# Optimization experiments

Hardware: AMD Instinct MI355X
Metric: run time of the kernel (lower is better)

Reference implementation:

```python
import jax, jax.numpy as jnp
import numpy as np

NUM_HEADS = 16
HEAD_SIZE = 64
HIDDEN = NUM_HEADS * HEAD_SIZE  # 1024


def setup_inputs() -> dict:
    key = jax.random.key(0)
    ks = jax.random.split(key, 9)
    B, S1, S2 = 8, 1024, 1024
    scale = 1.0 / np.sqrt(HIDDEN)
    inp = {
        "s1_hidden_states": jax.random.normal(ks[0], (B, S1, HIDDEN), jnp.float32),
        "s2_hidden_states": jax.random.normal(ks[1], (B, S2, HIDDEN), jnp.float32),
        "s2_attention_mask": jnp.zeros((B, 1, 1, S2), jnp.float32),
        "Wq": jax.random.normal(ks[2], (HIDDEN, HIDDEN), jnp.float32) * scale,
        "bq": jnp.zeros((HIDDEN,), jnp.float32),
        "Wk": jax.random.normal(ks[3], (HIDDEN, HIDDEN), jnp.float32) * scale,
        "bk": jnp.zeros((HIDDEN,), jnp.float32),
        "Wv": jax.random.normal(ks[4], (HIDDEN, HIDDEN), jnp.float32) * scale,
        "bv": jnp.zeros((HIDDEN,), jnp.float32),
        "cl_att": 1,
    }
    return inp


def _split_heads(x):
    # [B, S, H*D] -> [B, H, S, D]
    B, S, _ = x.shape
    return x.reshape(B, S, NUM_HEADS, HEAD_SIZE).transpose(0, 2, 1, 3)


def reference(s1_hidden_states, s2_hidden_states, s2_attention_mask,
              Wq, bq, Wk, bk, Wv, bv, cl_att):
    q = _split_heads(s1_hidden_states @ Wq + bq)  # [B,H,S1,D]
    k = _split_heads(s2_hidden_states @ Wk + bk)  # [B,H,S2,D]
    v = _split_heads(s2_hidden_states @ Wv + bv)  # [B,H,S2,D]

    scores = jnp.einsum("bhqd,bhkd->bhqk", q, k) / np.sqrt(HEAD_SIZE)
    scores = scores + s2_attention_mask  # broadcast [B,1,1,S2]
    probs = jax.nn.softmax(scores, axis=-1)
    if cl_att:
        probs = jax.nn.softmax(1.0 - probs + s2_attention_mask, axis=-1)
    # dropout is identity in eval/reference mode
    ctx = jnp.einsum("bhqk,bhkd->bhqd", probs, v)  # [B,H,S1,D]
    B, _, S1, _ = ctx.shape
    return ctx.transpose(0, 2, 1, 3).reshape(B, S1, HIDDEN)
```

## Files before the change

### kernel.cpp

```cpp
#include <hip/hip_runtime.h>
#include <hip/hip_bf16.h>

typedef unsigned short u16;
typedef __attribute__((ext_vector_type(8))) short bf16x8;
typedef __attribute__((ext_vector_type(4))) float f32x4;
typedef __attribute__((ext_vector_type(4))) unsigned u32x4;

#define L2E 1.4426950408889634f

__device__ __forceinline__ u16 f2bf(float f) {
  unsigned u = __float_as_uint(f);
  u = u + 0x7fffu + ((u >> 16) & 1u);
  return (u16)(u >> 16);
}
__device__ __forceinline__ unsigned cvtpk(float a, float b) {
  unsigned r;
  asm("v_cvt_pk_bf16_f32 %0, %1, %2" : "=v"(r) : "v"(a), "v"(b));
  return r;
}

__global__ void conv_f32_bf16(const float* __restrict__ in, u16* __restrict__ out, int n4) {
  int i = blockIdx.x * blockDim.x + threadIdx.x;
  int stride = gridDim.x * blockDim.x;
  for (; i < n4; i += stride) {
    float4 v = ((const float4*)in)[i];
    ushort4 o = make_ushort4(f2bf(v.x), f2bf(v.y), f2bf(v.z), f2bf(v.w));
    ((ushort4*)out)[i] = o;
  }
}

__global__ void wtrans3(const float* __restrict__ Wq, const float* __restrict__ Wk,
                        const float* __restrict__ Wv,
                        u16* __restrict__ Wtq, u16* __restrict__ Wtk, u16* __restrict__ Wtv) {
  int z = blockIdx.z;
  const float* W = (z == 0) ? Wq : (z == 1) ? Wk : Wv;
  u16* Wt = (z == 0) ? Wtq : (z == 1) ? Wtk : Wtv;
  __shared__ float T[32][33];
  int k0 = blockIdx.y * 32, n0 = blockIdx.x * 32;
  int tx = threadIdx.x, ty = threadIdx.y;
  #pragma unroll
  for (int j = 0; j < 4; ++j) T[ty + 8*j][tx] = W[(size_t)(k0 + ty + 8*j) * 1024 + n0 + tx];
  __syncthreads();
  #pragma unroll
  for (int j = 0; j < 4; ++j) Wt[(size_t)(n0 + ty + 8*j) * 1024 + k0 + tx] = f2bf(T[tx][ty + 8*j]);
}

__global__ __launch_bounds__(256) void qkv_gemm3(const u16* __restrict__ X1, const u16* __restrict__ X2,
                                                 const u16* __restrict__ Wtq, const u16* __restrict__ Wtk,
                                                 const u16* __restrict__ Wtv,
                                                 const float* __restrict__ bq, const float* __restrict__ bk,
                                                 const float* __restrict__ bv,
                                                 u16* __restrict__ Qo, u16* __restrict__ Ko, u16* __restrict__ Vo) {
  int z = blockIdx.z;
  const u16* X   = (z == 0) ? X1 : X2;
  const u16* Wt  = (z == 0) ? Wtq : (z == 1) ? Wtk : Wtv;
  const float* bias = (z == 0) ? bq : (z == 1) ? bk : bv;
  u16* outp = (z == 0) ? Qo : (z == 1) ? Ko : Vo;

  __shared__ __align__(16) u16 As[128 * 32];
  __shared__ __align__(16) u16 Bs[128 * 32];
  int tid = threadIdx.x;
  int m0 = blockIdx.y * 128, n0 = blockIdx.x * 128;
  int w = tid >> 6, l = tid & 63;
  int wm = w >> 1, wn = w & 1;
  const int4* Xs = (const int4*)X;
  const int4* Ws = (const int4*)Wt;
  int4* As4 = (int4*)As;
  int4* Bs4 = (int4*)Bs;
  f32x4 acc[4][4] = {};
  for (int kt = 0; kt < 32; ++kt) {
    #pragma unroll
    for (int c = 0; c < 2; ++c) {
      int i = c * 256 + tid;
      int row = i >> 2, kc = i & 3;
      __builtin_amdgcn_global_load_lds(
          (const __attribute__((address_space(1))) void*)&Xs[(size_t)(m0 + row) * 128 + kt * 4 + kc],
          (__attribute__((address_space(3))) void*)&As4[i], 16, 0, 0);
      __builtin_amdgcn_global_load_lds(
          (const __attribute__((address_space(1))) void*)&Ws[(size_t)(n0 + row) * 128 + kt * 4 + kc],
          (__attribute__((address_space(3))) void*)&Bs4[i], 16, 0, 0);
    }
    __syncthreads();
    bf16x8 a[4], bb[4];
    #pragma unroll
    for (int mc = 0; mc < 4; ++mc) a[mc]  = *(const bf16x8*)&As[(wm*64 + mc*16 + (l & 15)) * 32 + (l >> 4) * 8];
    #pragma unroll
    for (int nc = 0; nc < 4; ++nc) bb[nc] = *(const bf16x8*)&Bs[(wn*64 + nc*16 + (l & 15)) * 32 + (l >> 4) * 8];
    #pragma unroll
    for (int mc = 0; mc < 4; ++mc)
      #pragma unroll
      for (int nc = 0; nc < 4; ++nc)
        acc[mc][nc] = __builtin_amdgcn_mfma_f32_16x16x32_bf16(a[mc], bb[nc], acc[mc][nc], 0, 0, 0);
    __syncthreads();
  }
  #pragma unroll
  for (int nc = 0; nc < 4; ++nc) {
    int n = n0 + wn * 64 + nc * 16 + (l & 15);
    float bvv = bias[n];
    int h = n >> 6, d = n & 63;
    #pragma unroll
    for (int mc = 0; mc < 4; ++mc) {
      int srow_base = m0 + wm * 64 + mc * 16 + (l >> 4) * 4;
      if (z == 2) {
        int b = srow_base >> 10, s = srow_base & 1023;
        ushort4 vv;
        vv.x = f2bf(acc[mc][nc][0] + bvv);
        vv.y = f2bf(acc[mc][nc][1] + bvv);
        vv.z = f2bf(acc[mc][nc][2] + bvv);
        vv.w = f2bf(acc[mc][nc][3] + bvv);
        *(ushort4*)&outp[((size_t)((b * 16 + h) * 64 + d)) * 1024 + s] = vv;
      } else {
        #pragma unroll
        for (int r = 0; r < 4; ++r) {
          int sm = srow_base + r;
          int b = sm >> 10, s = sm & 1023;
          outp[((size_t)((b * 16 + h) * 1024 + s)) * 64 + d] = f2bf(acc[mc][nc][r] + bvv);
        }
      }
    }
  }
}

__global__ __launch_bounds__(256, 3) void attn12(const u16* __restrict__ Q, const u16* __restrict__ K,
                                                 const u16* __restrict__ Vt, const float* __restrict__ mask,
                                                 const int* __restrict__ clp, float* __restrict__ out) {
  __shared__ __align__(16) u16 KVl[2][8192];
  __shared__ __align__(16) float maskL2[1024];
  __shared__ float z1p[4][32];
  __shared__ float z2p[4][32];

  int bid = blockIdx.x;
  int xcd = bid & 7, idx = bid >> 3;
  int bh = xcd * 16 + (idx >> 5);
  int qt = idx & 31;
  int b = bh >> 4, h = bh & 15;
  int tid = threadIdx.x;
  int w = tid >> 6, l = tid & 63;
  int lq = l & 15, g = l >> 4;
  int qb = qt * 32;

  const u16* Kb = K + (size_t)bh * 65536;
  const u16* Vb = Vt + (size_t)bh * 65536;
  int cl = clp[0];

  const u16* kS[4]; int kD[4];
  #pragma unroll
  for (int c_ = 0; c_ < 4; ++c_) {
    int i_ = c_ * 256 + tid, row_ = i_ >> 3, ch_ = i_ & 7;
    int f_ = (row_ & 3) | ((((row_ >> 3) ^ (row_ >> 4)) & 1) << 2);
    kS[c_] = Kb + row_ * 64 + (ch_ ^ f_) * 8;
    kD[c_] = i_ * 8;
  }
  const u16* vS[4]; int vD[4];
  #pragma unroll
  for (int c_ = 0; c_ < 4; ++c_) {
    int i_ = c_ * 256 + tid, row_ = i_ >> 4, ch_ = i_ & 15;
    vS[c_] = Vb + row_ * 1024 + (ch_ ^ (row_ & 15)) * 8;
    vD[c_] = i_ * 8;
  }

#define STAGE_K(bi, t) do { _Pragma("unroll")                                                 \
    for (int c_ = 0; c_ < 4; ++c_)                                                           \
      __builtin_amdgcn_global_load_lds(                                                      \
        (const __attribute__((address_space(1))) void*)(kS[c_] + (t) * 8192),                \
        (__attribute__((address_space(3))) void*)&KVl[bi][kD[c_]], 16, 0, 0); } while (0)

#define STAGE_V(bi, t) do { _Pragma("unroll")                                                 \
    for (int c_ = 0; c_ < 4; ++c_)                                                           \
      __builtin_amdgcn_global_load_lds(                                                      \
        (const __attribute__((address_space(1))) void*)(vS[c_] + (t) * 128),                 \
        (__attribute__((address_space(3))) void*)&KVl[bi][vD[c_]], 16, 0, 0); } while (0)

  STAGE_K(0, 0);

  for (int i = tid; i < 1024; i += 256) maskL2[i] = mask[b * 1024 + i] * L2E;

  bf16x8 qf[2][2];
  #pragma unroll
  for (int qg = 0; qg < 2; ++qg) {
    const u16* Qp = Q + ((size_t)bh * 1024 + qb + qg * 16 + lq) * 64 + g * 8;
    qf[qg][0] = *(const bf16x8*)Qp;
    qf[qg][1] = *(const bf16x8*)(Qp + 32);
  }

  int kOff[2][2];
  #pragma unroll
  for (int c = 0; c < 2; ++c) {
    int row128 = w * 32 + ((lq >> 2) << 3) + c * 4 + (lq & 3);
    int F = (row128 & 3) | ((((row128 >> 3) ^ (row128 >> 4)) & 1) << 2);
    kOff[c][0] = row128 * 64 + ((g ^ F) * 8);
    kOff[c][1] = row128 * 64 + (((g + 4) ^ F) * 8);
  }
  int vOff[4];
  #pragma unroll
  for (int dc = 0; dc < 4; ++dc) {
    int row = dc * 16 + lq;
    vOff[dc] = row * 128 + (((w * 4 + g) ^ (row & 15)) * 8);
  }
  int mBase = w * 32 + g * 8;

  __syncthreads();

  const float sl2e = 0.125f * L2E;
  float z1[2] = {0.f, 0.f};
  int cur = 0;
  #pragma unroll
  for (int t = 0; t < 8; ++t) {
    if (t < 7) STAGE_K(cur ^ 1, t + 1);
    else       STAGE_K(0, 0);
    #pragma unroll
    for (int c = 0; c < 2; ++c) {
      bf16x8 kf0 = *(const bf16x8*)&KVl[cur][kOff[c][0]];
      bf16x8 kf1 = *(const bf16x8*)&KVl[cur][kOff[c][1]];
      const float4 mk = *(const float4*)&maskL2[t * 128 + mBase + c * 4];
      #pragma unroll
      for (int qg = 0; qg < 2; ++qg) {
        f32x4 tt = {0.f, 0.f, 0.f, 0.f};
        tt = __builtin_amdgcn_mfma_f32_16x16x32_bf16(kf0, qf[qg][0], tt, 0, 0, 0);
        tt = __builtin_amdgcn_mfma_f32_16x16x32_bf16(kf1, qf[qg][1], tt, 0, 0, 0);
        float e0 = __builtin_amdgcn_exp2f(fmaf(tt[0], sl2e, mk.x));
        float e1 = __builtin_amdgcn_exp2f(fmaf(tt[1], sl2e, mk.y));
        float e2 = __builtin_amdgcn_exp2f(fmaf(tt[2], sl2e, mk.z));
        float e3 = __builtin_amdgcn_exp2f(fmaf(tt[3], sl2e, mk.w));
        z1[qg] += (e0 + e1) + (e2 + e3);
      }
    }
    __syncthreads();
    cur ^= 1;
  }
  STAGE_V(1, 0);

  #pragma unroll
  for (int qg = 0; qg < 2; ++qg) {
    z1[qg] += __shfl_xor(z1[qg], 16);
    z1[qg] += __shfl_xor(z1[qg], 32);
  }
  if (l < 16) { z1p[w][l] = z1[0]; z1p[w][16 + l] = z1[1]; }
  __syncthreads();
  float lm[2];
  #pragma unroll
  for (int qg = 0; qg < 2; ++qg) {
    int q = qg * 16 + lq;
    lm[qg] = __builtin_amdgcn_logf(((z1p[0][q] + z1p[1][q]) + (z1p[2][q] + z1p[3][q])));
  }

  f32x4 acc[2][4] = {};
  float z2[2] = {0.f, 0.f};
  #pragma unroll
  for (int t = 0; t < 8; ++t) {
    u32x4 pk[2];
    #pragma unroll
    for (int c = 0; c < 2; ++c) {
      bf16x8 kf0 = *(const bf16x8*)&KVl[0][kOff[c][0]];
      bf16x8 kf1 = *(const bf16x8*)&KVl[0][kOff[c][1]];
      const float4 mk = *(const float4*)&maskL2[t * 128 + mBase + c * 4];
      #pragma unroll
      for (int qg = 0; qg < 2; ++qg) {
        f32x4 tt = {0.f, 0.f, 0.f, 0.f};
        tt = __builtin_amdgcn_mfma_f32_16x16x32_bf16(kf0, qf[qg][0], tt, 0, 0, 0);
        tt = __builtin_amdgcn_mfma_f32_16x16x32_bf16(kf1, qf[qg][1], tt, 0, 0, 0);
        float p10 = __builtin_amdgcn_exp2f(fmaf(tt[0], sl2e, mk.x) - lm[qg]);
        float p11 = __builtin_amdgcn_exp2f(fmaf(tt[1], sl2e, mk.y) - lm[qg]);
        float p12 = __builtin_amdgcn_exp2f(fmaf(tt[2], sl2e, mk.z) - lm[qg]);
        float p13 = __builtin_amdgcn_exp2f(fmaf(tt[3], sl2e, mk.w) - lm[qg]);
        if (cl) {
          float p20 = __builtin_amdgcn_exp2f(fmaf(-L2E, p10, mk.x));
          float p21 = __builtin_amdgcn_exp2f(fmaf(-L2E, p11, mk.y));
          float p22 = __builtin_amdgcn_exp2f(fmaf(-L2E, p12, mk.z));
          float p23 = __builtin_amdgcn_exp2f(fmaf(-L2E, p13, mk.w));
          z2[qg] += (p20 + p21) + (p22 + p23);
          pk[qg][c * 2 + 0] = cvtpk(p20, p21);
          pk[qg][c * 2 + 1] = cvtpk(p22, p23);
        } else {
          pk[qg][c * 2 + 0] = cvtpk(p10, p11);
          pk[qg][c * 2 + 1] = cvtpk(p12, p13);
        }
      }
    }
    #pragma unroll
    for (int dc = 0; dc < 4; ++dc) {
      bf16x8 vf = *(const bf16x8*)&KVl[1][vOff[dc]];
      #pragma unroll
      for (int qg = 0; qg < 2; ++qg)
        acc[qg][dc] = __builtin_amdgcn_mfma_f32_16x16x32_bf16(
            __builtin_bit_cast(bf16x8, pk[qg]), vf, acc[qg][dc], 0, 0, 0);
    }
    __syncthreads();
    if (t < 7) {
      STAGE_K(0, t + 1);
      STAGE_V(1, t + 1);
      __syncthreads();
    }
  }

  #pragma unroll
  for (int qg = 0; qg < 2; ++qg) {
    z2[qg] += __shfl_xor(z2[qg], 16);
    z2[qg] += __shfl_xor(z2[qg], 32);
  }
  if (l < 16) { z2p[w][l] = z2[0]; z2p[w][16 + l] = z2[1]; }
  float* redF = (float*)&KVl[0][0];
  if (w > 0) {
    #pragma unroll
    for (int qg = 0; qg < 2; ++qg)
      #pragma unroll
      for (int dc = 0; dc < 4; ++dc)
        #pragma unroll
        for (int r = 0; r < 4; ++r)
          redF[(w - 1) * 2176 + (qg * 16 + g * 4 + r) * 68 + dc * 16 + lq] = acc[qg][dc][r];
  }
  __syncthreads();
  if (w == 0) {
    #pragma unroll
    for (int qg = 0; qg < 2; ++qg) {
      #pragma unroll
      for (int r = 0; r < 4; ++r) {
        int q = qg * 16 + g * 4 + r;
        float Z2 = (z2p[0][q] + z2p[1][q]) + (z2p[2][q] + z2p[3][q]);
        float phi = cl ? __builtin_amdgcn_rcpf(Z2) : 1.0f;
        size_t orow = ((size_t)(b * 1024 + qb + q)) * 1024 + h * 64;
        #pragma unroll
        for (int dc = 0; dc < 4; ++dc) {
          int dq = q * 68 + dc * 16 + lq;
          float o = acc[qg][dc][r] + redF[dq] + redF[2176 + dq] + redF[4352 + dq];
          out[orow + dc * 16 + lq] = o * phi;
        }
      }
    }
  }
#undef STAGE_K
#undef STAGE_V
}

extern "C" void kernel_launch(void* const* d_in, const int* in_sizes, int n_in,
                              void* d_out, int out_size, void* d_ws, size_t ws_size,
                              hipStream_t stream) {
  const float* s1   = (const float*)d_in[0];
  const float* s2   = (const float*)d_in[1];
  const float* mask = (const float*)d_in[2];
  const float* Wq   = (const float*)d_in[3];
  const float* bq   = (const float*)d_in[4];
  const float* Wk   = (const float*)d_in[5];
  const float* bk   = (const float*)d_in[6];
  const float* Wv   = (const float*)d_in[7];
  const float* bv   = (const float*)d_in[8];
  const int*   cl   = (const int*)d_in[9];
  float* out = (float*)d_out;

  u16* ws  = (u16*)d_ws;
  const size_t M1 = 1024 * 1024;
  u16* X1  = ws;
  u16* X2  = ws + 8 * M1;
  u16* Wtq = ws + 16 * M1;
  u16* Wtk = Wtq + M1;
  u16* Wtv = Wtk + M1;
  u16* Qb  = Wtv + M1;
  u16* Kb  = Qb + 8 * M1;
  u16* Vtb = Kb + 8 * M1;

  conv_f32_bf16<<<2048, 256, 0, stream>>>(s1, X1, 2097152);
  conv_f32_bf16<<<2048, 256, 0, stream>>>(s2, X2, 2097152);
  wtrans3<<<dim3(32, 32, 3), dim3(32, 8), 0, stream>>>(Wq, Wk, Wv, Wtq, Wtk, Wtv);
  qkv_gemm3<<<dim3(8, 64, 3), 256, 0, stream>>>(X1, X2, Wtq, Wtk, Wtv, bq, bk, bv, Qb, Kb, Vtb);
  attn12<<<4096, 256, 0, stream>>>(Qb, Kb, Vtb, mask, cl, out);
}
```

Baseline: 212.6 us.

## Cache unnormalized score exponentials in registers instead of recomputing QK^T

The first pass over K now stores the exp'd scores as packed bf16 in a 64-entry register array. The second pass reuses them with a reciprocal of the row sum instead of redoing the QK^T MFMAs and exponentials. K staging in the second pass is dropped and V is double-buffered, so one barrier per tile is removed. This saves MFMA and exp work but costs many more VGPRs, which is why occupancy is lowered from 3 to 2 blocks. Using bf16-rounded probabilities before the second softmax adds some precision loss.

```diff
diff --git a/kernel.cpp b/kernel.cpp
--- a/kernel.cpp
+++ b/kernel.cpp
@@ -18,6 +18,8 @@
   asm("v_cvt_pk_bf16_f32 %0, %1, %2" : "=v"(r) : "v"(a), "v"(b));
   return r;
 }
+__device__ __forceinline__ float lo16(unsigned v) { return __uint_as_float(v << 16); }
+__device__ __forceinline__ float hi16(unsigned v) { return __uint_as_float(v & 0xffff0000u); }
 
 __global__ void conv_f32_bf16(const float* __restrict__ in, u16* __restrict__ out, int n4) {
   int i = blockIdx.x * blockDim.x + threadIdx.x;
@@ -121,7 +123,7 @@
   }
 }
 
-__global__ __launch_bounds__(256, 3) void attn12(const u16* __restrict__ Q, const u16* __restrict__ K,
+__global__ __launch_bounds__(256, 2) void attn13(const u16* __restrict__ Q, const u16* __restrict__ K,
                                                  const u16* __restrict__ Vt, const float* __restrict__ mask,
                                                  const int* __restrict__ clp, float* __restrict__ out) {
   __shared__ __align__(16) u16 KVl[2][8192];
@@ -202,12 +204,13 @@
   __syncthreads();
 
   const float sl2e = 0.125f * L2E;
+  unsigned sp[64];
   float z1[2] = {0.f, 0.f};
   int cur = 0;
   #pragma unroll
   for (int t = 0; t < 8; ++t) {
     if (t < 7) STAGE_K(cur ^ 1, t + 1);
-    else       STAGE_K(0, 0);
+    else       STAGE_V(0, 0);
     #pragma unroll
     for (int c = 0; c < 2; ++c) {
       bf16x8 kf0 = *(const bf16x8*)&KVl[cur][kOff[c][0]];
@@ -223,12 +226,13 @@
         float e2 = __builtin_amdgcn_exp2f(fmaf(tt[2], sl2e, mk.z));
         float e3 = __builtin_amdgcn_exp2f(fmaf(tt[3], sl2e, mk.w));
         z1[qg] += (e0 + e1) + (e2 + e3);
+        sp[t * 8 + qg * 4 + c * 2 + 0] = cvtpk(e0, e1);
+        sp[t * 8 + qg * 4 + c * 2 + 1] = cvtpk(e2, e3);
       }
     }
     __syncthreads();
     cur ^= 1;
   }
-  STAGE_V(1, 0);
 
   #pragma unroll
   for (int qg = 0; qg < 2; ++qg) {
@@ -237,60 +241,46 @@
   }
   if (l < 16) { z1p[w][l] = z1[0]; z1p[w][16 + l] = z1[1]; }
   __syncthreads();
-  float lm[2];
+  float cr[2];
   #pragma unroll
   for (int qg = 0; qg < 2; ++qg) {
     int q = qg * 16 + lq;
-    lm[qg] = __builtin_amdgcn_logf(((z1p[0][q] + z1p[1][q]) + (z1p[2][q] + z1p[3][q])));
+    float Z1 = (z1p[0][q] + z1p[1][q]) + (z1p[2][q] + z1p[3][q]);
+    cr[qg] = L2E * __builtin_amdgcn_rcpf(Z1);
   }
 
   f32x4 acc[2][4] = {};
   float z2[2] = {0.f, 0.f};
   #pragma unroll
   for (int t = 0; t < 8; ++t) {
+    if (t < 7) STAGE_V((t + 1) & 1, t + 1);
     u32x4 pk[2];
     #pragma unroll
-    for (int c = 0; c < 2; ++c) {
-      bf16x8 kf0 = *(const bf16x8*)&KVl[0][kOff[c][0]];
-      bf16x8 kf1 = *(const bf16x8*)&KVl[0][kOff[c][1]];
-      const float4 mk = *(const float4*)&maskL2[t * 128 + mBase + c * 4];
-      #pragma unroll
-      for (int qg = 0; qg < 2; ++qg) {
-        f32x4 tt = {0.f, 0.f, 0.f, 0.f};
-        tt = __builtin_amdgcn_mfma_f32_16x16x32_bf16(kf0, qf[qg][0], tt, 0, 0, 0);
-        tt = __builtin_amdgcn_mfma_f32_16x16x32_bf16(kf1, qf[qg][1], tt, 0, 0, 0);
-        float p10 = __builtin_amdgcn_exp2f(fmaf(tt[0], sl2e, mk.x) - lm[qg]);
-        float p11 = __builtin_amdgcn_exp2f(fmaf(tt[1], sl2e, mk.y) - lm[qg]);
-        float p12 = __builtin_amdgcn_exp2f(fmaf(tt[2], sl2e, mk.z) - lm[qg]);
-        float p13 = __builtin_amdgcn_exp2f(fmaf(tt[3], sl2e, mk.w) - lm[qg]);
-        if (cl) {
-          float p20 = __builtin_amdgcn_exp2f(fmaf(-L2E, p10, mk.x));
-          float p21 = __builtin_amdgcn_exp2f(fmaf(-L2E, p11, mk.y));
-          float p22 = __builtin_amdgcn_exp2f(fmaf(-L2E, p12, mk.z));
-          float p23 = __builtin_amdgcn_exp2f(fmaf(-L2E, p13, mk.w));
-          z2[qg] += (p20 + p21) + (p22 + p23);
-          pk[qg][c * 2 + 0] = cvtpk(p20, p21);
-          pk[qg][c * 2 + 1] = cvtpk(p22, p23);
-        } else {
-          pk[qg][c * 2 + 0] = cvtpk(p10, p11);
-          pk[qg][c * 2 + 1] = cvtpk(p12, p13);
+    for (int qg = 0; qg < 2; ++qg) {
+      if (cl) {
+        #pragma unroll
+        for (int j = 0; j < 4; ++j) {
+          unsigned e = sp[t * 8 + qg * 4 + j];
+          float mkA = maskL2[t * 128 + mBase + 2 * j];
+          float mkB = maskL2[t * 128 + mBase + 2 * j + 1];
+          float pA = __builtin_amdgcn_exp2f(fmaf(-cr[qg], lo16(e), mkA));
+          float pB = __builtin_amdgcn_exp2f(fmaf(-cr[qg], hi16(e), mkB));
+          z2[qg] += pA + pB;
+          pk[qg][j] = cvtpk(pA, pB);
         }
+      } else {
+        pk[qg] = *(u32x4*)&sp[t * 8 + qg * 4];
       }
     }
     #pragma unroll
     for (int dc = 0; dc < 4; ++dc) {
-      bf16x8 vf = *(const bf16x8*)&KVl[1][vOff[dc]];
+      bf16x8 vf = *(const bf16x8*)&KVl[t & 1][vOff[dc]];
       #pragma unroll
       for (int qg = 0; qg < 2; ++qg)
         acc[qg][dc] = __builtin_amdgcn_mfma_f32_16x16x32_bf16(
             __builtin_bit_cast(bf16x8, pk[qg]), vf, acc[qg][dc], 0, 0, 0);
     }
-    __syncthreads();
-    if (t < 7) {
-      STAGE_K(0, t + 1);
-      STAGE_V(1, t + 1);
-      __syncthreads();
-    }
+    if (t < 7) __syncthreads();
   }
 
   #pragma unroll
@@ -316,8 +306,14 @@
       #pragma unroll
       for (int r = 0; r < 4; ++r) {
         int q = qg * 16 + g * 4 + r;
-        float Z2 = (z2p[0][q] + z2p[1][q]) + (z2p[2][q] + z2p[3][q]);
-        float phi = cl ? __builtin_amdgcn_rcpf(Z2) : 1.0f;
+        float phi;
+        if (cl) {
+          float Z2 = (z2p[0][q] + z2p[1][q]) + (z2p[2][q] + z2p[3][q]);
+          phi = __builtin_amdgcn_rcpf(Z2);
+        } else {
+          float Z1 = (z1p[0][q] + z1p[1][q]) + (z1p[2][q] + z1p[3][q]);
+          phi = __builtin_amdgcn_rcpf(Z1);
+        }
         size_t orow = ((size_t)(b * 1024 + qb + q)) * 1024 + h * 64;
         #pragma unroll
         for (int dc = 0; dc < 4; ++dc) {
@@ -362,5 +358,5 @@
   conv_f32_bf16<<<2048, 256, 0, stream>>>(s2, X2, 2097152);
   wtrans3<<<dim3(32, 32, 3), dim3(32, 8), 0, stream>>>(Wq, Wk, Wv, Wtq, Wtk, Wtv);
   qkv_gemm3<<<dim3(8, 64, 3), 256, 0, stream>>>(X1, X2, Wtq, Wtk, Wtv, bq, bk, bv, Qb, Kb, Vtb);
-  attn12<<<4096, 256, 0, stream>>>(Qb, Kb, Vtb, mask, cl, out);
-}
+  attn13<<<4096, 256, 0, stream>>>(Qb, Kb, Vtb, mask, cl, out);
+}
```

Result: faster. 187.5 us (-11.8%).
